# Optimization experiments

Measured on AMD Instinct MI355X. Metric: run time of the kernel, lower is better.

The kernel has to match this reference:

```python
import jax, jax.numpy as jnp
import numpy as np

B, U, H, W, C, F = 4, 81, 64, 64, 4, 32  # batch, angres^2 views, height, width, channels, n_filters


def setup_inputs() -> dict:
    key = jax.random.key(0)
    k1, k2 = jax.random.split(key)
    lfi = jax.random.normal(k1, (B, U, H, W, C), dtype=jnp.float32)
    f_maps = jax.random.uniform(k2, (B, H, W, F), dtype=jnp.float32)
    return {"lfi": lfi, "f_maps": f_maps}


def reference(lfi, f_maps):
    # height cue: per (b, filter) mean over the h axis -> length-w vector,
    # normalized by its max (h == w so it broadcasts along the h axis of lfi)
    hv = jnp.mean(f_maps, axis=1)                      # [B, W, F]
    hv = hv / jnp.max(hv, axis=1, keepdims=True)       # normalize per (b, f)
    h_mask = jnp.transpose(hv, (0, 2, 1))              # [B, F, H]
    # original: stack over filters of lfi * mask (broadcast on h axis),
    # then reduce_mean over channel axis. Mask is channel-independent, so
    # reduce channels first to avoid the [B,F,U,H,W,C] intermediate.
    lfi_mean = jnp.mean(lfi, axis=4)                   # [B, U, H, W]
    out = jnp.einsum('buyx,bfy->buyxf', lfi_mean, h_mask)  # [B, U, H, W, F]
    return out
```

## Files before the change

kernel.cpp:

```cpp
#include <hip/hip_runtime.h>
#include <hip/hip_bf16.h>

#define BB 4
#define UU 81
#define HH 64
#define WW 64
#define CC 4
#define FF 32

typedef float fx4 __attribute__((ext_vector_type(4)));

__global__ __launch_bounds__(1024) void mask_kernel(
    const float* __restrict__ fmaps, float* __restrict__ mask) {
    const int b = blockIdx.x;
    const int t = threadIdx.x;
    __shared__ float hv[WW * FF];
    const float* fb = fmaps + (size_t)b * HH * WW * FF;

    float v[2];
#pragma unroll
    for (int r = 0; r < 2; ++r) {
        const int idx = t + r * 1024;
        float s = 0.f;
#pragma unroll 4
        for (int h = 0; h < HH; ++h) s += fb[h * WW * FF + idx];
        v[r] = s * (1.f / HH);
        hv[idx] = v[r];
    }
    __syncthreads();

    for (int s = WW / 2; s > 0; s >>= 1) {
#pragma unroll
        for (int r = 0; r < 2; ++r) {
            const int idx = t + r * 1024;
            const int w = idx / FF, f = idx % FF;
            if (w < s) hv[idx] = fmaxf(hv[idx], hv[(w + s) * FF + f]);
        }
        __syncthreads();
    }

#pragma unroll
    for (int r = 0; r < 2; ++r) {
        const int idx = t + r * 1024;
        const int f = idx & (FF - 1);
        mask[(size_t)b * WW * FF + idx] = v[r] / hv[f];
    }
}

#define NPT 8
__global__ __launch_bounds__(256) void out_kernel(
    const fx4* __restrict__ lfi4,
    const fx4* __restrict__ mask4,
    fx4* __restrict__ out4) {
    const int b = blockIdx.y;
    const fx4* __restrict__ lfiB  = lfi4  + (size_t)b * UU * HH * WW;
    const fx4* __restrict__ maskB = mask4 + (size_t)b * WW * (FF / 4);
    fx4* __restrict__ outB        = out4  + (size_t)b * UU * HH * WW * (FF / 4);

    const size_t base = (size_t)blockIdx.x * (256 * NPT) + threadIdx.x;

    fx4 lf[NPT];
    fx4 mk[NPT];
#pragma unroll
    for (int k = 0; k < NPT; ++k) {
        const size_t idx = base + (size_t)k * 256;
        const int f4 = (int)(idx & 7);
        const size_t rest = idx >> 3;
        const int y = (int)((rest >> 6) & 63);
        lf[k] = lfiB[rest];
        mk[k] = maskB[y * 8 + f4];
    }
#pragma unroll
    for (int k = 0; k < NPT; ++k) {
        const size_t idx = base + (size_t)k * 256;
        const float m = (lf[k].x + lf[k].y + lf[k].z + lf[k].w) * 0.25f;
        fx4 o = m * mk[k];
        __builtin_nontemporal_store(o, &outB[idx]);
    }
}

extern "C" void kernel_launch(void* const* d_in, const int* in_sizes, int n_in,
                              void* d_out, int out_size, void* d_ws, size_t ws_size,
                              hipStream_t stream) {
    const float* lfi = (const float*)d_in[0];
    const float* fmaps = (const float*)d_in[1];
    float* out = (float*)d_out;
    float* mask = (float*)d_ws;

    mask_kernel<<<BB, 1024, 0, stream>>>(fmaps, mask);

    const size_t perB4 = (size_t)UU * HH * WW * (FF / 4);
    const int grid_x = (int)(perB4 / (256 * NPT));
    dim3 grid(grid_x, BB);
    out_kernel<<<grid, 256, 0, stream>>>(
        (const fx4*)lfi, (const fx4*)mask, (fx4*)out);
}
```

Measured before the change: 209.6 us.

## Split mask computation into parallel partial sums and simplify out-kernel indexing

The single 4-block mask kernel becomes two kernels. The first spreads the mean over h across 16 blocks that write partial sums to workspace, and the second combines the partials, runs the max-reduce and normalizes. The output kernel now computes its row, filter and y indices once per thread and loads only four mask vectors, since consecutive k steps share a y every two iterations. This adds a kernel launch and a workspace round trip in return for more parallelism in the mask stage and less index arithmetic.

```diff
diff --git a/kernel.cpp b/kernel.cpp
--- a/kernel.cpp
+++ b/kernel.cpp
@@ -10,40 +10,58 @@
 
 typedef float fx4 __attribute__((ext_vector_type(4)));
 
-__global__ __launch_bounds__(1024) void mask_kernel(
-    const float* __restrict__ fmaps, float* __restrict__ mask) {
-    const int b = blockIdx.x;
+#define WS_PARTIAL 0
+#define WS_MASK 32768
+
+__global__ __launch_bounds__(1024) void mask_partial_kernel(
+    const float* __restrict__ fmaps, float* __restrict__ ws) {
+    const int hs = blockIdx.x;
+    const int b = blockIdx.y;
     const int t = threadIdx.x;
-    __shared__ float hv[WW * FF];
-    const float* fb = fmaps + (size_t)b * HH * WW * FF;
+    const float* fb = fmaps + (size_t)b * HH * WW * FF + (size_t)hs * 16 * WW * FF;
+    float* part = ws + WS_PARTIAL + ((size_t)b * 4 + hs) * (WW * FF);
 
-    float v[2];
 #pragma unroll
     for (int r = 0; r < 2; ++r) {
         const int idx = t + r * 1024;
         float s = 0.f;
-#pragma unroll 4
-        for (int h = 0; h < HH; ++h) s += fb[h * WW * FF + idx];
-        v[r] = s * (1.f / HH);
-        hv[idx] = v[r];
+#pragma unroll
+        for (int h = 0; h < 16; ++h) s += fb[h * WW * FF + idx];
+        part[idx] = s;
+    }
+}
+
+__global__ __launch_bounds__(256) void mask_norm_kernel(
+    const float* __restrict__ ws_in, float* __restrict__ mask) {
+    const int b = blockIdx.x;
+    const int t = threadIdx.x;
+    __shared__ float sm[WW * FF];
+    const float* part = ws_in + WS_PARTIAL + (size_t)b * 4 * (WW * FF);
+
+    float v[8];
+#pragma unroll
+    for (int j = 0; j < 8; ++j) {
+        const int i = t + 256 * j;
+        float s = part[i] + part[WW * FF + i] + part[2 * WW * FF + i] +
+                  part[3 * WW * FF + i];
+        v[j] = s * (1.f / HH);
+        sm[i] = v[j];
     }
     __syncthreads();
 
     for (int s = WW / 2; s > 0; s >>= 1) {
 #pragma unroll
-        for (int r = 0; r < 2; ++r) {
-            const int idx = t + r * 1024;
-            const int w = idx / FF, f = idx % FF;
-            if (w < s) hv[idx] = fmaxf(hv[idx], hv[(w + s) * FF + f]);
+        for (int j = 0; j < 8; ++j) {
+            const int i = t + 256 * j;
+            const int w = i >> 5;
+            if (w < s) sm[i] = fmaxf(sm[i], sm[i + s * FF]);
         }
         __syncthreads();
     }
-
 #pragma unroll
-    for (int r = 0; r < 2; ++r) {
-        const int idx = t + r * 1024;
-        const int f = idx & (FF - 1);
-        mask[(size_t)b * WW * FF + idx] = v[r] / hv[f];
+    for (int j = 0; j < 8; ++j) {
+        const int i = t + 256 * j;
+        mask[(size_t)b * WW * FF + i] = v[j] / sm[i & (FF - 1)];
     }
 }
 
@@ -58,24 +76,24 @@
     fx4* __restrict__ outB        = out4  + (size_t)b * UU * HH * WW * (FF / 4);
 
     const size_t base = (size_t)blockIdx.x * (256 * NPT) + threadIdx.x;
+    const size_t r0 = base >> 3;
+    const int f4 = (int)(base & 7);
+    const int y0 = (int)((r0 >> 6) & 63);
+
+    fx4 mk[NPT / 2];
+#pragma unroll
+    for (int j = 0; j < NPT / 2; ++j)
+        mk[j] = maskB[((y0 + j) & 63) * 8 + f4];
 
     fx4 lf[NPT];
-    fx4 mk[NPT];
+#pragma unroll
+    for (int k = 0; k < NPT; ++k) lf[k] = lfiB[r0 + (size_t)k * 32];
+
 #pragma unroll
     for (int k = 0; k < NPT; ++k) {
-        const size_t idx = base + (size_t)k * 256;
-        const int f4 = (int)(idx & 7);
-        const size_t rest = idx >> 3;
-        const int y = (int)((rest >> 6) & 63);
-        lf[k] = lfiB[rest];
-        mk[k] = maskB[y * 8 + f4];
-    }
-#pragma unroll
-    for (int k = 0; k < NPT; ++k) {
-        const size_t idx = base + (size_t)k * 256;
         const float m = (lf[k].x + lf[k].y + lf[k].z + lf[k].w) * 0.25f;
-        fx4 o = m * mk[k];
-        __builtin_nontemporal_store(o, &outB[idx]);
+        fx4 o = m * mk[k >> 1];
+        __builtin_nontemporal_store(o, &outB[base + (size_t)k * 256]);
     }
 }
 
@@ -85,9 +103,11 @@
     const float* lfi = (const float*)d_in[0];
     const float* fmaps = (const float*)d_in[1];
     float* out = (float*)d_out;
-    float* mask = (float*)d_ws;
+    float* ws = (float*)d_ws;
+    float* mask = ws + WS_MASK;
 
-    mask_kernel<<<BB, 1024, 0, stream>>>(fmaps, mask);
+    mask_partial_kernel<<<dim3(4, BB), 1024, 0, stream>>>(fmaps, ws);
+    mask_norm_kernel<<<BB, 256, 0, stream>>>(ws, mask);
 
     const size_t perB4 = (size_t)UU * HH * WW * (FF / 4);
     const int grid_x = (int)(perB4 / (256 * NPT));
```

Result: faster. 200.5 us (-4.4%).
